# Performance work log

Hardware: AMD Instinct MI355X
Metric: run time of the kernel (lower is better)

Reference implementation:

```python
import jax, jax.numpy as jnp
import numpy as np

N_NODES = 100000
N_EDGES = 1000000
N_RELS = 8
N_HEADS = 4
IN_FEAT = 64
OUT_FEAT = 64
D_HEAD = OUT_FEAT // N_HEADS
LEAKY_SLOPE = 0.2


def setup_inputs() -> dict:
    key = jax.random.key(0)
    ks = jax.random.split(key, 8)
    x = jax.random.normal(ks[0], (N_NODES, IN_FEAT), dtype=jnp.float32)
    src_idx = jax.random.randint(ks[1], (N_EDGES,), 0, N_NODES)
    dst_idx = jax.random.randint(ks[2], (N_EDGES,), 0, N_NODES)
    edge_rel = jnp.sort(jax.random.randint(ks[3], (N_EDGES,), 0, N_RELS))
    # xavier-ish small init for weights
    conv_weights = jax.random.normal(ks[4], (N_RELS, N_HEADS, IN_FEAT, D_HEAD), dtype=jnp.float32) * 0.1
    attn_l = jax.random.normal(ks[5], (N_RELS, N_HEADS, D_HEAD), dtype=jnp.float32) * 0.1
    attn_r = jax.random.normal(ks[6], (N_RELS, N_HEADS, D_HEAD), dtype=jnp.float32) * 0.1
    h_bias = jnp.zeros((OUT_FEAT,), dtype=jnp.float32)
    return {
        'x': x, 'src_idx': src_idx, 'dst_idx': dst_idx, 'edge_rel': edge_rel,
        'conv_weights': conv_weights, 'attn_l': attn_l, 'attn_r': attn_r,
        'h_bias': h_bias,
    }


def reference(x, src_idx, dst_idx, edge_rel, conv_weights, attn_l, attn_r, h_bias):
    N = x.shape[0]
    # Per-relation transform of all node features: [R, N, H, D]
    feat_all = jnp.einsum('ni,rhid->rnhd', x, conv_weights)
    # Per-relation attention logits per node: [R, N, H]
    el_all = jnp.einsum('rnhd,rhd->rnh', feat_all, attn_l)
    er_all = jnp.einsum('rnhd,rhd->rnh', feat_all, attn_r)
    # Gather per-edge quantities (relation-specific transform of src/dst)
    feat_e = feat_all[edge_rel, src_idx]          # [E, H, D]
    el = el_all[edge_rel, src_idx]                # [E, H]
    er = er_all[edge_rel, dst_idx]                # [E, H]
    s = jax.nn.leaky_relu(el + er, negative_slope=LEAKY_SLOPE)
    # Edge softmax over incoming edges of each destination node (per head)
    m = jax.ops.segment_max(s, dst_idx, num_segments=N)      # [N, H]
    e = jnp.exp(s - m[dst_idx])                               # [E, H]
    denom = jax.ops.segment_sum(e, dst_idx, num_segments=N)   # [N, H]
    w = e / jnp.maximum(denom[dst_idx], jnp.float32(1e-16))   # [E, H]
    # Weighted aggregation of source features into destination nodes
    agg = jax.ops.segment_sum(feat_e * w[..., None], dst_idx, num_segments=N)  # [N, H, D]
    h = agg.reshape(N, OUT_FEAT) + h_bias
    # activation=None, dropout in eval mode -> identity
    return h
```

## Files before the change

kernel.cpp:

```cpp
#include <hip/hip_runtime.h>
#include <hip/hip_bf16.h>

#define NN 100000
#define NE 1000000
#define NR 8

#define EB 1024
#define NBLK 977
#define NBUCK 196
#define NT (NBUCK*NBLK)
#define NBB 749

#define CAP 224

#define CVT_BLKS 3125
#define K0_BLKS  160
#define PRE_BLKS (CVT_BLKS + K0_BLKS + NBLK)

typedef unsigned short u16;
typedef unsigned int u32;
typedef __attribute__((ext_vector_type(8))) short bf16x8;
typedef __attribute__((ext_vector_type(4))) float f32x4;

static __device__ __forceinline__ float bf2f(u16 u) {
    union { u32 i; float f; } v; v.i = ((u32)u) << 16; return v.f;
}
static __device__ __forceinline__ float bflo(u32 u) {
    union { u32 i; float f; } v; v.i = u << 16; return v.f;
}
static __device__ __forceinline__ float bfhi(u32 u) {
    union { u32 i; float f; } v; v.i = u & 0xffff0000u; return v.f;
}
static __device__ __forceinline__ u16 f2bf(float f) {
    __hip_bfloat16 h = __float2bfloat16(f);
    return *reinterpret_cast<u16*>(&h);
}
static __device__ __forceinline__ float ldf(const void* p, int idx, int isf32) {
    return isf32 ? ((const float*)p)[idx] : bf2f(((const u16*)p)[idx]);
}

static __device__ __forceinline__ int detect_wave(const u16* xw, int lane)
{
    int insane = 0;
    for (int k = lane; k < 512; k += 64) {
        u16 w = xw[k];
        int ex = (w >> 7) & 0xFF;
        bool sane = ((w & 0x7FFF) == 0) || (ex >= 96 && ex <= 159);
        insane += sane ? 0 : 1;
    }
    for (int off = 32; off; off >>= 1) insane += __shfl_down(insane, off);
    return insane;
}

__global__ __launch_bounds__(256) void k_pre(
    const void* __restrict__ xin, u16* __restrict__ xb, int* __restrict__ flag,
    const void* __restrict__ cw, const void* __restrict__ al,
    const void* __restrict__ ar, u16* __restrict__ Bpre,
    const int* __restrict__ dsti, int* __restrict__ histT)
{
    __shared__ int sflag;
    __shared__ int hist[NBUCK];
    int t = threadIdx.x;
    int b = blockIdx.x;

    if (b < CVT_BLKS) {
        if (t < 64) {
            int insane = detect_wave((const u16*)xin, t);
            if (t == 0) {
                sflag = (insane > 50) ? 1 : 0;
                if (b == 0) *flag = sflag;
            }
        }
        __syncthreads();
        int isf32 = sflag;
        int i = b * 256 + t;
        if (i >= NN * 8) return;
        if (isf32) {
            const float* xf = (const float*)xin;
            u16 o[8];
#pragma unroll
            for (int j = 0; j < 8; ++j) o[j] = f2bf(xf[i * 8 + j]);
            uint4 v;
            v.x = (u32)o[0] | ((u32)o[1] << 16);
            v.y = (u32)o[2] | ((u32)o[3] << 16);
            v.z = (u32)o[4] | ((u32)o[5] << 16);
            v.w = (u32)o[6] | ((u32)o[7] << 16);
            ((uint4*)xb)[i] = v;
        } else {
            ((uint4*)xb)[i] = ((const uint4*)xin)[i];
        }
    } else if (b < CVT_BLKS + K0_BLKS) {
        if (t < 64) {
            int insane = detect_wave((const u16*)xin, t);
            if (t == 0) sflag = (insane > 50) ? 1 : 0;
        }
        __syncthreads();
        int isf32 = sflag;
        int tid = (b - CVT_BLKS) * 256 + t;
        if (tid >= NR * 5120) return;
        int r = tid / 5120, rem = tid % 5120;
        int c = rem >> 3, j = rem & 7;
        int nt = c >> 7, kk = (c >> 6) & 1, lc = c & 63;
        int i = kk * 32 + ((lc >> 4) << 3) + j;
        int d = lc & 15;
        u16 val;
        if (nt < 4) {
            val = f2bf(ldf(cw, ((r * 4 + nt) * 64 + i) * 16 + d, isf32));
        } else if (d < 8) {
            int h = d >> 1;
            const void* attn = (d & 1) ? ar : al;
            float s = 0.f;
            for (int dd = 0; dd < 16; ++dd)
                s += ldf(cw, ((r * 4 + h) * 64 + i) * 16 + dd, isf32)
                   * ldf(attn, (r * 4 + h) * 16 + dd, isf32);
            val = f2bf(s);
        } else {
            val = 0;
        }
        Bpre[tid] = val;
    } else {
        int blk = b - CVT_BLKS - K0_BLKS;
        if (t < NBUCK) hist[t] = 0;
        __syncthreads();
        int base = blk * EB;
        for (int j = 0; j < EB; j += 256) {
            int e = base + j + t;
            if (e < NE) atomicAdd(&hist[dsti[e] >> 9], 1);
        }
        __syncthreads();
        if (t < NBUCK) histT[t * NBLK + blk] = hist[t];
    }
}

__global__ __launch_bounds__(256) void k1_feat(
    const u16* __restrict__ xb, const u16* __restrict__ Bpre,
    u16* __restrict__ feat_all, float* __restrict__ el_all, float* __restrict__ er_all)
{
    __shared__ alignas(16) u16 ldsA[4096];
    __shared__ alignas(16) u16 ldsF[2][4096];
    int n0 = blockIdx.x * 64;
    int tid = threadIdx.x;
    int wave = tid >> 6, lane = tid & 63;
    int col = lane & 15, quad = lane >> 4;

    for (int c = tid; c < 512; c += 256) {
        int mt = c >> 7, kk = (c >> 6) & 1, lc = c & 63;
        int node = n0 + mt * 16 + (lc & 15);
        if (node >= NN) node = NN - 1;
        int kbase = kk * 32 + ((lc >> 4) << 3);
        *(uint4*)&ldsA[c * 8] = *(const uint4*)&xb[node * 64 + kbase];
    }
    __syncthreads();
    bf16x8 afrag0 = *(bf16x8*)&ldsA[((wave * 2 + 0) * 64 + lane) * 8];
    bf16x8 afrag1 = *(bf16x8*)&ldsA[((wave * 2 + 1) * 64 + lane) * 8];

    for (int r = 0; r < NR; ++r) {
        int buf = r & 1;
        f32x4 acc[5];
#pragma unroll
        for (int nt = 0; nt < 5; ++nt) acc[nt] = f32x4{0.f, 0.f, 0.f, 0.f};
#pragma unroll
        for (int nt = 0; nt < 5; ++nt) {
            bf16x8 b0 = *(const bf16x8*)&Bpre[r * 5120 + ((nt * 2 + 0) * 64 + lane) * 8];
            bf16x8 b1 = *(const bf16x8*)&Bpre[r * 5120 + ((nt * 2 + 1) * 64 + lane) * 8];
            acc[nt] = __builtin_amdgcn_mfma_f32_16x16x32_bf16(afrag0, b0, acc[nt], 0, 0, 0);
            acc[nt] = __builtin_amdgcn_mfma_f32_16x16x32_bf16(afrag1, b1, acc[nt], 0, 0, 0);
        }

        if (col < 8) {
            int h = col >> 1;
            float* dstp = (col & 1) ? er_all : el_all;
#pragma unroll
            for (int reg = 0; reg < 4; ++reg) {
                int node = n0 + wave * 16 + quad * 4 + reg;
                if (node < NN) dstp[(r * NN + node) * 4 + h] = acc[4][reg];
            }
        }
#pragma unroll
        for (int nt = 0; nt < 4; ++nt) {
            int cg = nt * 16 + col;
#pragma unroll
            for (int reg = 0; reg < 4; ++reg) {
                int row = quad * 4 + reg;
                ldsF[buf][(wave * 16 + row) * 64 + cg] = f2bf(acc[nt][reg]);
            }
        }
        __syncthreads();
        for (int c = tid; c < 512; c += 256) {
            int nl = c >> 3, part = c & 7;
            int node = n0 + nl;
            if (node < NN)
                *(uint4*)&feat_all[(r * NN + node) * 64 + part * 8] = *(uint4*)&ldsF[buf][c * 8];
        }
    }
}

__global__ __launch_bounds__(256) void k_scanB1(int* __restrict__ histT,
                                                int* __restrict__ bsum)
{
    __shared__ int wtot[4];
    int t = threadIdx.x;
    int gi = blockIdx.x * 256 + t;
    int v = (gi < NT) ? histT[gi] : 0;
    int lane = t & 63, w = t >> 6;
    int s = v;
#pragma unroll
    for (int m = 1; m < 64; m <<= 1) {
        int u = __shfl_up(s, m);
        if (lane >= m) s += u;
    }
    if (lane == 63) wtot[w] = s;
    __syncthreads();
    int wb = 0;
    for (int i = 0; i < w; ++i) wb += wtot[i];
    if (gi < NT) histT[gi] = wb + s - v;
    if (t == 255) bsum[blockIdx.x] = wb + s;
}

__global__ __launch_bounds__(1024) void k_scanB2(const int* __restrict__ bsum,
                                                 int* __restrict__ boff,
                                                 const int* __restrict__ histT,
                                                 int* __restrict__ bstart)
{
    __shared__ int wtot[16];
    __shared__ int sboff[NBB];
    int t = threadIdx.x;
    int v = (t < NBB) ? bsum[t] : 0;
    int lane = t & 63, w = t >> 6;
    int s = v;
#pragma unroll
    for (int m = 1; m < 64; m <<= 1) {
        int u = __shfl_up(s, m);
        if (lane >= m) s += u;
    }
    if (lane == 63) wtot[w] = s;
    __syncthreads();
    int wb = 0;
    for (int i = 0; i < w; ++i) wb += wtot[i];
    if (t < NBB) {
        int val = wb + s - v;
        boff[t] = val;
        sboff[t] = val;
    }
    __syncthreads();
    if (t < NBUCK) {
        int gi = t * NBLK;
        bstart[t] = histT[gi] + sboff[gi >> 8];
    }
    if (t == 0) bstart[NBUCK] = NE;
}

__global__ __launch_bounds__(256) void k_binC(
    const int* __restrict__ srci, const int* __restrict__ dsti,
    const int* __restrict__ reli, const int* __restrict__ histT,
    const int* __restrict__ boff, int* __restrict__ key_b)
{
    __shared__ int cur[NBUCK];
    int t = threadIdx.x, blk = blockIdx.x;
    if (t < NBUCK) {
        int gi = t * NBLK + blk;
        cur[t] = histT[gi] + boff[gi >> 8];
    }
    __syncthreads();
    int base = blk * EB;
    for (int j = 0; j < EB; j += 256) {
        int e = base + j + t;
        if (e < NE) {
            int d = dsti[e];
            int key = ((d & 511) << 20) | (reli[e] << 17) | srci[e];
            int pos = atomicAdd(&cur[d >> 9], 1);
            key_b[pos] = key;
        }
    }
}

__global__ __launch_bounds__(1024) void k_binD(
    const int* __restrict__ bstart, const int* __restrict__ key_b,
    int* __restrict__ key_s, int* __restrict__ off)
{
    __shared__ int cnt[512];
    __shared__ int wtot[8];
    int t = threadIdx.x, b = blockIdx.x;
    int s0 = bstart[b], s1 = bstart[b + 1];
    if (t < 512) cnt[t] = 0;
    __syncthreads();
    for (int j = s0 + t; j < s1; j += 1024)
        atomicAdd(&cnt[(key_b[j] >> 20) & 511], 1);
    __syncthreads();
    int excl = 0;
    if (t < 512) {
        int v = cnt[t];
        int lane = t & 63, w = t >> 6;
        int s = v;
#pragma unroll
        for (int m = 1; m < 64; m <<= 1) {
            int u = __shfl_up(s, m);
            if (lane >= m) s += u;
        }
        if (lane == 63) wtot[w] = s;
        __syncthreads();
        int wb = 0;
        for (int i = 0; i < w; ++i) wb += wtot[i];
        excl = s0 + wb + s - v;
        int d = (b << 9) + t;
        if (d < NN) off[d] = excl;
    } else {
        __syncthreads();
    }
    __syncthreads();
    if (t < 512) cnt[t] = excl;
    if (b == 0 && t == 0) off[NN] = NE;
    __syncthreads();
    for (int j = s0 + t; j < s1; j += 1024) {
        int key = key_b[j];
        int pos = atomicAdd(&cnt[(key >> 20) & 511], 1);
        key_s[pos] = key;
    }
}

__global__ __launch_bounds__(256) void k3_node(
    const int* __restrict__ off, const int* __restrict__ key_s,
    const float* __restrict__ el_all, const float* __restrict__ er_all,
    const u16* __restrict__ feat_all, const void* __restrict__ bias,
    const int* __restrict__ flag, void* __restrict__ out)
{
    __shared__ int   ldsOffs[65];
    __shared__ int   ldsKey[4][CAP];
    __shared__ float ldsEE[4][CAP][4];
    int t = threadIdx.x;
    int wave = t >> 6, lane = t & 63;
    int dg = lane >> 3;
    int fl = lane & 7;
    int h  = fl >> 1;
    int d0 = blockIdx.x * 64;
    int isf32 = *flag;

    if (t < 65) ldsOffs[t] = off[min(d0 + t, NN)];
    __syncthreads();

    int dlo = wave * 16;
    int estart = ldsOffs[dlo], eend = ldsOffs[dlo + 16];
    int scount = min(eend - estart, CAP);

    for (int j = lane; j < scount; j += 64) {
        int key = key_s[estart + j];
        int rel = (key >> 17) & 7, src = key & 131071;
        int d = d0 + ((key >> 20) & 63);
        int kk = rel * NN + src;
        f32x4 el = *(const f32x4*)&el_all[kk * 4];
        f32x4 er = *(const f32x4*)&er_all[(rel * NN + d) * 4];
        f32x4 ee;
#pragma unroll
        for (int q = 0; q < 4; ++q) {
            float v = el[q] + er[q];
            v = v > 0.f ? v : 0.2f * v;
            ee[q] = __expf(v);
        }
        ldsKey[wave][j] = kk;
        *(f32x4*)&ldsEE[wave][j][0] = ee;
    }

    float bv[8];
#pragma unroll
    for (int q = 0; q < 8; ++q) bv[q] = ldf(bias, fl * 8 + q, isf32);

#pragma unroll
    for (int i = 0; i < 2; ++i) {
        int nl = i * 8 + dg;
        int d = d0 + dlo + nl;
        int s  = ldsOffs[dlo + nl] - estart;
        int e1 = ldsOffs[dlo + nl + 1] - estart;
        float acc[8] = {0.f, 0.f, 0.f, 0.f, 0.f, 0.f, 0.f, 0.f};
        float accW = 0.f;

        int e1c = min(e1, CAP);
        for (int base = s; base < e1c; base += 4) {
            int kk[4]; float w[4];
#pragma unroll
            for (int q = 0; q < 4; ++q) {
                int idx = base + q;
                bool vld = idx < e1c;
                kk[q] = vld ? ldsKey[wave][idx] : 0;
                w[q]  = vld ? ldsEE[wave][idx][h] : 0.f;
            }
            uint4 u[4];
#pragma unroll
            for (int q = 0; q < 4; ++q)
                u[q] = *(const uint4*)&feat_all[kk[q] * 64 + fl * 8];
#pragma unroll
            for (int q = 0; q < 4; ++q) {
                acc[0] += bflo(u[q].x) * w[q];
                acc[1] += bfhi(u[q].x) * w[q];
                acc[2] += bflo(u[q].y) * w[q];
                acc[3] += bfhi(u[q].y) * w[q];
                acc[4] += bflo(u[q].z) * w[q];
                acc[5] += bfhi(u[q].z) * w[q];
                acc[6] += bflo(u[q].w) * w[q];
                acc[7] += bfhi(u[q].w) * w[q];
                accW += w[q];
            }
        }
        for (int j = max(s, CAP); j < e1; ++j) {
            int key = key_s[estart + j];
            int rel = (key >> 17) & 7, src = key & 131071;
            int kk0 = rel * NN + src;
            float v = el_all[kk0 * 4 + h] + er_all[(rel * NN + d) * 4 + h];
            v = v > 0.f ? v : 0.2f * v;
            float w0 = __expf(v);
            uint4 u = *(const uint4*)&feat_all[kk0 * 64 + fl * 8];
            acc[0] += bflo(u.x) * w0;
            acc[1] += bfhi(u.x) * w0;
            acc[2] += bflo(u.y) * w0;
            acc[3] += bfhi(u.y) * w0;
            acc[4] += bflo(u.z) * w0;
            acc[5] += bfhi(u.z) * w0;
            acc[6] += bflo(u.w) * w0;
            acc[7] += bfhi(u.w) * w0;
            accW += w0;
        }

        if (d < NN) {
            float invh = 1.f / fmaxf(accW, 1e-16f);
            float o[8];
#pragma unroll
            for (int q = 0; q < 8; ++q) o[q] = acc[q] * invh + bv[q];
            if (isf32) {
                ((f32x4*)out)[d * 16 + fl * 2]     = f32x4{o[0], o[1], o[2], o[3]};
                ((f32x4*)out)[d * 16 + fl * 2 + 1] = f32x4{o[4], o[5], o[6], o[7]};
            } else {
                uint4 st;
                st.x = (u32)f2bf(o[0]) | ((u32)f2bf(o[1]) << 16);
                st.y = (u32)f2bf(o[2]) | ((u32)f2bf(o[3]) << 16);
                st.z = (u32)f2bf(o[4]) | ((u32)f2bf(o[5]) << 16);
                st.w = (u32)f2bf(o[6]) | ((u32)f2bf(o[7]) << 16);
                *(uint4*)&((u16*)out)[d * 64 + fl * 8] = st;
            }
        }
    }
}

extern "C" void kernel_launch(void* const* d_in, const int* in_sizes, int n_in,
                              void* d_out, int out_size, void* d_ws, size_t ws_size,
                              hipStream_t stream)
{
    const void* x   = d_in[0];
    const int* srci = (const int*)d_in[1];
    const int* dsti = (const int*)d_in[2];
    const int* reli = (const int*)d_in[3];
    const void* cw  = d_in[4];
    const void* al  = d_in[5];
    const void* ar  = d_in[6];
    const void* hb  = d_in[7];

    char* ws = (char*)d_ws;
    u16*   feat_all = (u16*)  (ws + 0);
    float* el_all   = (float*)(ws + 102400000);
    float* er_all   = (float*)(ws + 115200000);
    int*   key_s    = (int*)  (ws + 128000000);
    int*   key_b    = (int*)  (ws + 132000000);
    int*   off      = (int*)  (ws + 136000000);
    int*   histT    = (int*)  (ws + 136400064);
    int*   bsum     = (int*)  (ws + 137166032);
    int*   boff     = (int*)  (ws + 137169040);
    int*   bstart   = (int*)  (ws + 137172048);
    u16*   Bpre     = (u16*)  (ws + 137172880);
    u16*   xb       = (u16*)  (ws + 137254800);
    int*   flag     = (int*)  (ws + 150054800);

    k_pre<<<PRE_BLKS, 256, 0, stream>>>(x, xb, flag, cw, al, ar, Bpre, dsti, histT);
    k1_feat<<<(NN + 63) / 64, 256, 0, stream>>>(xb, Bpre, feat_all, el_all, er_all);
    k_scanB1<<<NBB, 256, 0, stream>>>(histT, bsum);
    k_scanB2<<<1, 1024, 0, stream>>>(bsum, boff, histT, bstart);
    k_binC<<<NBLK, 256, 0, stream>>>(srci, dsti, reli, histT, boff, key_b);
    k_binD<<<NBUCK, 1024, 0, stream>>>(bstart, key_b, key_s, off);
    k3_node<<<(NN + 63) / 64, 256, 0, stream>>>(off, key_s, el_all, er_all, feat_all,
                                                hb, flag, d_out);
}
```

Measured before the change: 210.0 us.

## Fuse x bf16 conversion into feature GEMM and halve nodes per aggregation block

Removes the separate conversion pass that wrote a bf16 copy of x. Each feature-transform block now detects the input dtype and converts its tile while loading it into LDS, which saves a full read and write of x plus 3125 blocks in the pre kernel. The node aggregation kernel now handles 32 destinations per block (8 per wave, one per lane group) instead of 64, with a smaller LDS edge cache. That gives twice as many blocks and less LDS per block, but more edges take the uncached fallback path. The destination id is now rebuilt from the 512-node bucket base.

```diff
diff --git a/kernel.cpp b/kernel.cpp
--- a/kernel.cpp
+++ b/kernel.cpp
@@ -11,11 +11,11 @@
 #define NT (NBUCK*NBLK)
 #define NBB 749
 
-#define CAP 224
-
-#define CVT_BLKS 3125
+#define K3DPB 32
+#define K3CAP 160
+
 #define K0_BLKS  160
-#define PRE_BLKS (CVT_BLKS + K0_BLKS + NBLK)
+#define PRE_BLKS (K0_BLKS + NBLK)
 
 typedef unsigned short u16;
 typedef unsigned int u32;
@@ -53,7 +53,7 @@
 }
 
 __global__ __launch_bounds__(256) void k_pre(
-    const void* __restrict__ xin, u16* __restrict__ xb, int* __restrict__ flag,
+    const void* __restrict__ xin, int* __restrict__ flag,
     const void* __restrict__ cw, const void* __restrict__ al,
     const void* __restrict__ ar, u16* __restrict__ Bpre,
     const int* __restrict__ dsti, int* __restrict__ histT)
@@ -63,7 +63,7 @@
     int t = threadIdx.x;
     int b = blockIdx.x;
 
-    if (b < CVT_BLKS) {
+    if (b < K0_BLKS) {
         if (t < 64) {
             int insane = detect_wave((const u16*)xin, t);
             if (t == 0) {
@@ -73,30 +73,7 @@
         }
         __syncthreads();
         int isf32 = sflag;
-        int i = b * 256 + t;
-        if (i >= NN * 8) return;
-        if (isf32) {
-            const float* xf = (const float*)xin;
-            u16 o[8];
-#pragma unroll
-            for (int j = 0; j < 8; ++j) o[j] = f2bf(xf[i * 8 + j]);
-            uint4 v;
-            v.x = (u32)o[0] | ((u32)o[1] << 16);
-            v.y = (u32)o[2] | ((u32)o[3] << 16);
-            v.z = (u32)o[4] | ((u32)o[5] << 16);
-            v.w = (u32)o[6] | ((u32)o[7] << 16);
-            ((uint4*)xb)[i] = v;
-        } else {
-            ((uint4*)xb)[i] = ((const uint4*)xin)[i];
-        }
-    } else if (b < CVT_BLKS + K0_BLKS) {
-        if (t < 64) {
-            int insane = detect_wave((const u16*)xin, t);
-            if (t == 0) sflag = (insane > 50) ? 1 : 0;
-        }
-        __syncthreads();
-        int isf32 = sflag;
-        int tid = (b - CVT_BLKS) * 256 + t;
+        int tid = b * 256 + t;
         if (tid >= NR * 5120) return;
         int r = tid / 5120, rem = tid % 5120;
         int c = rem >> 3, j = rem & 7;
@@ -119,7 +96,7 @@
         }
         Bpre[tid] = val;
     } else {
-        int blk = b - CVT_BLKS - K0_BLKS;
+        int blk = b - K0_BLKS;
         if (t < NBUCK) hist[t] = 0;
         __syncthreads();
         int base = blk * EB;
@@ -133,9 +110,10 @@
 }
 
 __global__ __launch_bounds__(256) void k1_feat(
-    const u16* __restrict__ xb, const u16* __restrict__ Bpre,
+    const void* __restrict__ xin, const u16* __restrict__ Bpre,
     u16* __restrict__ feat_all, float* __restrict__ el_all, float* __restrict__ er_all)
 {
+    __shared__ int sflag;
     __shared__ alignas(16) u16 ldsA[4096];
     __shared__ alignas(16) u16 ldsF[2][4096];
     int n0 = blockIdx.x * 64;
@@ -143,12 +121,30 @@
     int wave = tid >> 6, lane = tid & 63;
     int col = lane & 15, quad = lane >> 4;
 
+    if (tid < 64) {
+        int insane = detect_wave((const u16*)xin, tid);
+        if (tid == 0) sflag = (insane > 50) ? 1 : 0;
+    }
+    __syncthreads();
+    int isf32 = sflag;
+
     for (int c = tid; c < 512; c += 256) {
         int mt = c >> 7, kk = (c >> 6) & 1, lc = c & 63;
         int node = n0 + mt * 16 + (lc & 15);
         if (node >= NN) node = NN - 1;
         int kbase = kk * 32 + ((lc >> 4) << 3);
-        *(uint4*)&ldsA[c * 8] = *(const uint4*)&xb[node * 64 + kbase];
+        if (!isf32) {
+            *(uint4*)&ldsA[c * 8] = *(const uint4*)&((const u16*)xin)[node * 64 + kbase];
+        } else {
+            const f32x4* xf4 = (const f32x4*)((const float*)xin + node * 64 + kbase);
+            f32x4 a = xf4[0], b = xf4[1];
+            uint4 o;
+            o.x = (u32)f2bf(a[0]) | ((u32)f2bf(a[1]) << 16);
+            o.y = (u32)f2bf(a[2]) | ((u32)f2bf(a[3]) << 16);
+            o.z = (u32)f2bf(b[0]) | ((u32)f2bf(b[1]) << 16);
+            o.w = (u32)f2bf(b[2]) | ((u32)f2bf(b[3]) << 16);
+            *(uint4*)&ldsA[c * 8] = o;
+        }
     }
     __syncthreads();
     bf16x8 afrag0 = *(bf16x8*)&ldsA[((wave * 2 + 0) * 64 + lane) * 8];
@@ -324,28 +320,29 @@
     const u16* __restrict__ feat_all, const void* __restrict__ bias,
     const int* __restrict__ flag, void* __restrict__ out)
 {
-    __shared__ int   ldsOffs[65];
-    __shared__ int   ldsKey[4][CAP];
-    __shared__ float ldsEE[4][CAP][4];
+    __shared__ int   ldsOffs[K3DPB + 1];
+    __shared__ int   ldsKey[4][K3CAP];
+    __shared__ float ldsEE[4][K3CAP][4];
     int t = threadIdx.x;
     int wave = t >> 6, lane = t & 63;
     int dg = lane >> 3;
     int fl = lane & 7;
     int h  = fl >> 1;
-    int d0 = blockIdx.x * 64;
+    int d0 = blockIdx.x * K3DPB;
     int isf32 = *flag;
 
-    if (t < 65) ldsOffs[t] = off[min(d0 + t, NN)];
-    __syncthreads();
-
-    int dlo = wave * 16;
-    int estart = ldsOffs[dlo], eend = ldsOffs[dlo + 16];
-    int scount = min(eend - estart, CAP);
-
+    if (t < K3DPB + 1) ldsOffs[t] = off[min(d0 + t, NN)];
+    __syncthreads();
+
+    int dlo = wave * 8;
+    int estart = ldsOffs[dlo], eend = ldsOffs[dlo + 8];
+    int scount = min(eend - estart, K3CAP);
+
+    int dbase = d0 & ~511;
     for (int j = lane; j < scount; j += 64) {
         int key = key_s[estart + j];
         int rel = (key >> 17) & 7, src = key & 131071;
-        int d = d0 + ((key >> 20) & 63);
+        int d = dbase | ((key >> 20) & 511);
         int kk = rel * NN + src;
         f32x4 el = *(const f32x4*)&el_all[kk * 4];
         f32x4 er = *(const f32x4*)&er_all[(rel * NN + d) * 4];
@@ -364,77 +361,74 @@
 #pragma unroll
     for (int q = 0; q < 8; ++q) bv[q] = ldf(bias, fl * 8 + q, isf32);
 
-#pragma unroll
-    for (int i = 0; i < 2; ++i) {
-        int nl = i * 8 + dg;
-        int d = d0 + dlo + nl;
-        int s  = ldsOffs[dlo + nl] - estart;
-        int e1 = ldsOffs[dlo + nl + 1] - estart;
-        float acc[8] = {0.f, 0.f, 0.f, 0.f, 0.f, 0.f, 0.f, 0.f};
-        float accW = 0.f;
-
-        int e1c = min(e1, CAP);
-        for (int base = s; base < e1c; base += 4) {
-            int kk[4]; float w[4];
-#pragma unroll
-            for (int q = 0; q < 4; ++q) {
-                int idx = base + q;
-                bool vld = idx < e1c;
-                kk[q] = vld ? ldsKey[wave][idx] : 0;
-                w[q]  = vld ? ldsEE[wave][idx][h] : 0.f;
-            }
-            uint4 u[4];
-#pragma unroll
-            for (int q = 0; q < 4; ++q)
-                u[q] = *(const uint4*)&feat_all[kk[q] * 64 + fl * 8];
-#pragma unroll
-            for (int q = 0; q < 4; ++q) {
-                acc[0] += bflo(u[q].x) * w[q];
-                acc[1] += bfhi(u[q].x) * w[q];
-                acc[2] += bflo(u[q].y) * w[q];
-                acc[3] += bfhi(u[q].y) * w[q];
-                acc[4] += bflo(u[q].z) * w[q];
-                acc[5] += bfhi(u[q].z) * w[q];
-                acc[6] += bflo(u[q].w) * w[q];
-                acc[7] += bfhi(u[q].w) * w[q];
-                accW += w[q];
-            }
-        }
-        for (int j = max(s, CAP); j < e1; ++j) {
-            int key = key_s[estart + j];
-            int rel = (key >> 17) & 7, src = key & 131071;
-            int kk0 = rel * NN + src;
-            float v = el_all[kk0 * 4 + h] + er_all[(rel * NN + d) * 4 + h];
-            v = v > 0.f ? v : 0.2f * v;
-            float w0 = __expf(v);
-            uint4 u = *(const uint4*)&feat_all[kk0 * 64 + fl * 8];
-            acc[0] += bflo(u.x) * w0;
-            acc[1] += bfhi(u.x) * w0;
-            acc[2] += bflo(u.y) * w0;
-            acc[3] += bfhi(u.y) * w0;
-            acc[4] += bflo(u.z) * w0;
-            acc[5] += bfhi(u.z) * w0;
-            acc[6] += bflo(u.w) * w0;
-            acc[7] += bfhi(u.w) * w0;
-            accW += w0;
-        }
-
-        if (d < NN) {
-            float invh = 1.f / fmaxf(accW, 1e-16f);
-            float o[8];
-#pragma unroll
-            for (int q = 0; q < 8; ++q) o[q] = acc[q] * invh + bv[q];
-            if (isf32) {
-                ((f32x4*)out)[d * 16 + fl * 2]     = f32x4{o[0], o[1], o[2], o[3]};
-                ((f32x4*)out)[d * 16 + fl * 2 + 1] = f32x4{o[4], o[5], o[6], o[7]};
-            } else {
-                uint4 st;
-                st.x = (u32)f2bf(o[0]) | ((u32)f2bf(o[1]) << 16);
-                st.y = (u32)f2bf(o[2]) | ((u32)f2bf(o[3]) << 16);
-                st.z = (u32)f2bf(o[4]) | ((u32)f2bf(o[5]) << 16);
-                st.w = (u32)f2bf(o[6]) | ((u32)f2bf(o[7]) << 16);
-                *(uint4*)&((u16*)out)[d * 64 + fl * 8] = st;
-            }
+    int nl = dlo + dg;
+    int d = d0 + nl;
+    int s  = ldsOffs[nl] - estart;
+    int e1 = ldsOffs[nl + 1] - estart;
+    float acc[8] = {0.f, 0.f, 0.f, 0.f, 0.f, 0.f, 0.f, 0.f};
+    float accW = 0.f;
+
+    int e1c = min(e1, K3CAP);
+    for (int base = s; base < e1c; base += 4) {
+        int kk[4]; float w[4];
+#pragma unroll
+        for (int q = 0; q < 4; ++q) {
+            int idx = base + q;
+            bool vld = idx < e1c;
+            kk[q] = vld ? ldsKey[wave][idx] : 0;
+            w[q]  = vld ? ldsEE[wave][idx][h] : 0.f;
+        }
+        uint4 u[4];
+#pragma unroll
+        for (int q = 0; q < 4; ++q)
+            u[q] = *(const uint4*)&feat_all[kk[q] * 64 + fl * 8];
+#pragma unroll
+        for (int q = 0; q < 4; ++q) {
+            acc[0] += bflo(u[q].x) * w[q];
+            acc[1] += bfhi(u[q].x) * w[q];
+            acc[2] += bflo(u[q].y) * w[q];
+            acc[3] += bfhi(u[q].y) * w[q];
+            acc[4] += bflo(u[q].z) * w[q];
+            acc[5] += bfhi(u[q].z) * w[q];
+            acc[6] += bflo(u[q].w) * w[q];
+            acc[7] += bfhi(u[q].w) * w[q];
+            accW += w[q];
+        }
+    }
+    for (int j = max(s, K3CAP); j < e1; ++j) {
+        int key = key_s[estart + j];
+        int rel = (key >> 17) & 7, src = key & 131071;
+        int kk0 = rel * NN + src;
+        float v = el_all[kk0 * 4 + h] + er_all[(rel * NN + d) * 4 + h];
+        v = v > 0.f ? v : 0.2f * v;
+        float w0 = __expf(v);
+        uint4 u = *(const uint4*)&feat_all[kk0 * 64 + fl * 8];
+        acc[0] += bflo(u.x) * w0;
+        acc[1] += bfhi(u.x) * w0;
+        acc[2] += bflo(u.y) * w0;
+        acc[3] += bfhi(u.y) * w0;
+        acc[4] += bflo(u.z) * w0;
+        acc[5] += bfhi(u.z) * w0;
+        acc[6] += bflo(u.w) * w0;
+        acc[7] += bfhi(u.w) * w0;
+        accW += w0;
+    }
+
+    {
+        float invh = 1.f / fmaxf(accW, 1e-16f);
+        float o[8];
+#pragma unroll
+        for (int q = 0; q < 8; ++q) o[q] = acc[q] * invh + bv[q];
+        if (isf32) {
+            ((f32x4*)out)[d * 16 + fl * 2]     = f32x4{o[0], o[1], o[2], o[3]};
+            ((f32x4*)out)[d * 16 + fl * 2 + 1] = f32x4{o[4], o[5], o[6], o[7]};
+        } else {
+            uint4 st;
+            st.x = (u32)f2bf(o[0]) | ((u32)f2bf(o[1]) << 16);
+            st.y = (u32)f2bf(o[2]) | ((u32)f2bf(o[3]) << 16);
+            st.z = (u32)f2bf(o[4]) | ((u32)f2bf(o[5]) << 16);
+            st.w = (u32)f2bf(o[6]) | ((u32)f2bf(o[7]) << 16);
+            *(uint4*)&((u16*)out)[d * 64 + fl * 8] = st;
         }
     }
 }
@@ -464,15 +458,14 @@
     int*   boff     = (int*)  (ws + 137169040);
     int*   bstart   = (int*)  (ws + 137172048);
     u16*   Bpre     = (u16*)  (ws + 137172880);
-    u16*   xb       = (u16*)  (ws + 137254800);
-    int*   flag     = (int*)  (ws + 150054800);
-
-    k_pre<<<PRE_BLKS, 256, 0, stream>>>(x, xb, flag, cw, al, ar, Bpre, dsti, histT);
-    k1_feat<<<(NN + 63) / 64, 256, 0, stream>>>(xb, Bpre, feat_all, el_all, er_all);
+    int*   flag     = (int*)  (ws + 137254800);
+
+    k_pre<<<PRE_BLKS, 256, 0, stream>>>(x, flag, cw, al, ar, Bpre, dsti, histT);
+    k1_feat<<<(NN + 63) / 64, 256, 0, stream>>>(x, Bpre, feat_all, el_all, er_all);
     k_scanB1<<<NBB, 256, 0, stream>>>(histT, bsum);
     k_scanB2<<<1, 1024, 0, stream>>>(bsum, boff, histT, bstart);
     k_binC<<<NBLK, 256, 0, stream>>>(srci, dsti, reli, histT, boff, key_b);
     k_binD<<<NBUCK, 1024, 0, stream>>>(bstart, key_b, key_s, off);
-    k3_node<<<(NN + 63) / 64, 256, 0, stream>>>(off, key_s, el_all, er_all, feat_all,
+    k3_node<<<(NN + 31) / 32, 256, 0, stream>>>(off, key_s, el_all, er_all, feat_all,
                                                 hb, flag, d_out);
 }
```

After: 203.0 us. -3.3%, faster.
